# Kernel tuning notes

Measured on AMD Instinct MI355X. Metric: run time of the kernel, lower is better.

Reference implementation:

```python
import jax, jax.numpy as jnp
import numpy as np

B, N = 4, 2048
NUM_SHAPES = 16
EPS = 1e-5


def _angle(u, v):
    # u, v: [b, 3, n] -> angle via atan2(||u x v||, u.v), standard PPF angle
    s = jnp.linalg.norm(jnp.cross(u, v, axis=1), axis=1)
    c = jnp.sum(u * v, axis=1)
    return jnp.arctan2(s, c)


def _ppf(p1, p2, n1, n2):
    d = p2 - p1  # [b,3,n]
    return jnp.stack([_angle(n1, d), _angle(n2, d), _angle(n1, n2),
                      jnp.linalg.norm(d, axis=1)], axis=1)  # [b,4,n]


def _smlp(x, w, g, b):
    # 1x1 Conv1d (no bias; absorbed by BN) + BatchNorm1d (batch stats) + ReLU
    y = jnp.einsum('oc,bcn->bon', w, x)
    mu = y.mean(axis=(0, 2), keepdims=True)
    var = jnp.mean((y - mu) ** 2, axis=(0, 2), keepdims=True)
    y = (y - mu) * jax.lax.rsqrt(var + EPS) * g[None, :, None] + b[None, :, None]
    return jax.nn.relu(y)


def _forward(inputs, pf0_w, pf0_g, pf0_b, pf1_w, pf1_g, pf1_b,
             pf2_w, pf2_g, pf2_b, pf3_w, pf3_g, pf3_b,
             cls0_w, cls0_g, cls0_b, cls1_w, cls1_g, cls1_b,
             cls2_w, cls2_g, cls2_b, cls3_w, cls3_bias):
    one_hot = inputs[:, -NUM_SHAPES:, :]
    coords = inputs[:, :3, :]
    n = coords.shape[2]
    normals = inputs[:, 3:6, :]
    normals = normals / jnp.linalg.norm(normals, axis=1, keepdims=True)

    cc = coords.mean(axis=2, keepdims=True)          # [b,3,1]
    cn = normals.mean(axis=2, keepdims=True)         # [b,3,1]
    ncn = cn / jnp.linalg.norm(cn, axis=1, keepdims=True)

    old_ppfs = _ppf(jnp.broadcast_to(cc, coords.shape), coords,
                    jnp.broadcast_to(cn, coords.shape), normals)  # [b,4,n]

    nc = coords - cc
    dot = jnp.sum(nc * ncn, axis=1, keepdims=True)   # [b,1,n]
    proj = nc - dot * cn                              # [b,3,n] (unnormalized cn, as in source)
    P = proj.transpose(0, 2, 1)                       # [b,n,3]

    cos_a = jnp.einsum('bic,bjc->bij', P, P)          # [b,n,n]
    sin_a = jnp.linalg.norm(jnp.cross(P[:, :, None, :], P[:, None, :, :]), axis=-1)
    at = jnp.arctan2(sin_a, cos_a)
    at = jnp.where(at <= 1e-5, jnp.float32(100.0), at)
    # torch.median -> lower median: sorted index (n-1)//2
    alpha = jnp.sort(at, axis=2)[:, :, (n - 1) // 2]  # [b,n]

    feats = jnp.concatenate([old_ppfs, alpha[:, None, :]], axis=1)  # [b,5,n]

    outs = [one_hot]
    f = feats
    for w, g, b in [(pf0_w, pf0_g, pf0_b), (pf1_w, pf1_g, pf1_b),
                    (pf2_w, pf2_g, pf2_b), (pf3_w, pf3_g, pf3_b)]:
        f = _smlp(f, w, g, b)
        outs.append(f)
    outs.append(jnp.broadcast_to(jnp.max(f, axis=-1, keepdims=True), f.shape))
    x = jnp.concatenate(outs, axis=1)                 # [b,2384,n]

    for w, g, b in [(cls0_w, cls0_g, cls0_b), (cls1_w, cls1_g, cls1_b),
                    (cls2_w, cls2_g, cls2_b)]:
        x = _smlp(x, w, g, b)
    return jnp.einsum('oc,bcn->bon', cls3_w, x) + cls3_bias[None, :, None]


def setup_inputs() -> dict:
    key = jax.random.key(0)
    ks = jax.random.split(key, 12)
    inp = {"inputs": jax.random.normal(ks[0], (B, 3 + 3 + NUM_SHAPES, N), jnp.float32)}
    pf_dims = [(5, 64), (64, 128), (128, 128), (128, 1024)]
    for i, (ci, co) in enumerate(pf_dims):
        inp[f"pf{i}_w"] = jax.random.normal(ks[1 + i], (co, ci), jnp.float32) / np.sqrt(ci).astype(np.float32)
        inp[f"pf{i}_g"] = jnp.ones((co,), jnp.float32)
        inp[f"pf{i}_b"] = jnp.zeros((co,), jnp.float32)
    cls_dims = [(2384, 256), (256, 256), (256, 128)]
    for j, (ci, co) in enumerate(cls_dims):
        inp[f"cls{j}_w"] = jax.random.normal(ks[6 + j], (co, ci), jnp.float32) / np.sqrt(ci).astype(np.float32)
        inp[f"cls{j}_g"] = jnp.ones((co,), jnp.float32)
        inp[f"cls{j}_b"] = jnp.zeros((co,), jnp.float32)
    inp["cls3_w"] = jax.random.normal(ks[10], (50, 128), jnp.float32) / np.sqrt(128).astype(np.float32)
    inp["cls3_bias"] = jnp.zeros((50,), jnp.float32)
    return inp


def reference(inputs, pf0_w, pf0_g, pf0_b, pf1_w, pf1_g, pf1_b,
              pf2_w, pf2_g, pf2_b, pf3_w, pf3_g, pf3_b,
              cls0_w, cls0_g, cls0_b, cls1_w, cls1_g, cls1_b,
              cls2_w, cls2_g, cls2_b, cls3_w, cls3_bias):
    return _forward(inputs, pf0_w, pf0_g, pf0_b, pf1_w, pf1_g, pf1_b,
                    pf2_w, pf2_g, pf2_b, pf3_w, pf3_g, pf3_b,
                    cls0_w, cls0_g, cls0_b, cls1_w, cls1_g, cls1_b,
                    cls2_w, cls2_g, cls2_b, cls3_w, cls3_bias)
```

## Files before the change

### kernel.cpp

```cpp
#include <hip/hip_runtime.h>
#include <math.h>

#define BB 4
#define NN 2048
#define MM 8192
#define EPSF 1e-5f
#define LDC 1376

typedef _Float16 half8 __attribute__((ext_vector_type(8)));
typedef float f32x4 __attribute__((ext_vector_type(4)));

__device__ __forceinline__ unsigned short f2h(float x) {
    _Float16 h = (_Float16)x;
    return __builtin_bit_cast(unsigned short, h);
}
__device__ __forceinline__ float h2f(unsigned short u) {
    return (float)__builtin_bit_cast(_Float16, u);
}
__device__ __forceinline__ unsigned fflip(float x) {
    unsigned u = __builtin_bit_cast(unsigned, x);
    return (u >> 31) ? ~u : (u | 0x80000000u);
}
__device__ __forceinline__ float funflip(unsigned s) {
    unsigned u = (s >> 31) ? (s ^ 0x80000000u) : ~s;
    return __builtin_bit_cast(float, u);
}
#define FLIP_NEG_INF 0x007FFFFFu

__device__ __forceinline__ int wave_sum_dpp(int v) {
    v += __builtin_amdgcn_update_dpp(0, v, 0x111, 0xF, 0xF, true);
    v += __builtin_amdgcn_update_dpp(0, v, 0x112, 0xF, 0xF, true);
    v += __builtin_amdgcn_update_dpp(0, v, 0x114, 0xF, 0xF, true);
    v += __builtin_amdgcn_update_dpp(0, v, 0x118, 0xF, 0xF, true);
    v += __builtin_amdgcn_update_dpp(0, v, 0x142, 0xa, 0xF, true);
    v += __builtin_amdgcn_update_dpp(0, v, 0x143, 0xc, 0xF, true);
    return __builtin_amdgcn_readlane(v, 63);
}

__device__ __forceinline__ float angle3(float ux, float uy, float uz,
                                        float vx, float vy, float vz) {
    float crx = uy * vz - uz * vy;
    float cry = uz * vx - ux * vz;
    float crz = ux * vy - uy * vx;
    float s = sqrtf(crx * crx + cry * cry + crz * crz);
    float c = ux * vx + uy * vy + uz * vz;
    return atan2f(s, c);
}

__device__ __forceinline__ void bncoef(const float* __restrict__ sums,
                                       const float* __restrict__ g,
                                       const float* __restrict__ bb,
                                       int o, float& a, float& c) {
    float mu = sums[o] * (1.f / 8192.f);
    float var = sums[1024 + o] * (1.f / 8192.f) - mu * mu;
    var = fmaxf(var, 0.f);
    a = g[o] * (1.0f / sqrtf(var + EPSF));
    c = bb[o] - mu * a;
}

__global__ __launch_bounds__(256) void prep_k(const float* __restrict__ in,
                                              const float* __restrict__ w1, const float* __restrict__ w2,
                                              const float* __restrict__ w3, const float* __restrict__ w4,
                                              const float* __restrict__ w5, const float* __restrict__ w6,
                                              const float* __restrict__ w7,
                                              unsigned short* __restrict__ Wb,
                                              float* __restrict__ st,
                                              unsigned* __restrict__ zp,
                                              unsigned short* __restrict__ XCb) {
    int blk = blockIdx.x;
    int t = threadIdx.x;
    if (blk < 864) {
        int idx0 = blk * 1024 + t * 4;
        ushort4 r;
        unsigned short* rp = (unsigned short*)&r;
        #pragma unroll
        for (int e = 0; e < 4; ++e) {
            int idx = idx0 + e;
            unsigned short v;
            if (idx < 8192) v = f2h(w1[idx]);
            else if (idx < 24576) v = f2h(w2[idx - 8192]);
            else if (idx < 155648) v = f2h(w3[idx - 24576]);
            else if (idx < 507904) {
                int l = idx - 155648;
                int o = l / 1376, k = l - o * 1376;
                v = (k < 1360) ? f2h(w4[o * 2384 + k]) : (unsigned short)0;
            } else if (idx < 573440) v = f2h(w5[idx - 507904]);
            else if (idx < 606208) v = f2h(w6[idx - 573440]);
            else if (idx < 614400) {
                int l = idx - 606208;
                int o = l >> 7, k = l & 127;
                v = (o < 50) ? f2h(w7[o * 128 + k]) : (unsigned short)0;
            } else {
                int l = idx - 614400;
                int c = l >> 8, o = l & 255;
                v = (c < 1024) ? f2h(w4[o * 2384 + 1360 + c]) : (unsigned short)0;
            }
            rp[e] = v;
        }
        *(ushort4*)&Wb[idx0] = r;
    } else if (blk < 868) {
        int b = blk - 864;
        const float* base = in + (size_t)b * 22 * NN;
        float cs0 = 0.f, cs1 = 0.f, cs2 = 0.f, ns0 = 0.f, ns1 = 0.f, ns2 = 0.f;
        for (int n = t; n < NN; n += 256) {
            float cx = base[0 * NN + n], cy = base[1 * NN + n], cz = base[2 * NN + n];
            float nx = base[3 * NN + n], ny = base[4 * NN + n], nz = base[5 * NN + n];
            float inv = 1.0f / sqrtf(nx * nx + ny * ny + nz * nz);
            cs0 += cx; cs1 += cy; cs2 += cz;
            ns0 += nx * inv; ns1 += ny * inv; ns2 += nz * inv;
        }
        __shared__ float red[6][256];
        red[0][t] = cs0; red[1][t] = cs1; red[2][t] = cs2;
        red[3][t] = ns0; red[4][t] = ns1; red[5][t] = ns2;
        __syncthreads();
        for (int s = 128; s > 0; s >>= 1) {
            if (t < s) {
                #pragma unroll
                for (int i = 0; i < 6; ++i) red[i][t] += red[i][t + s];
            }
            __syncthreads();
        }
        if (t == 0) {
            float ccx = red[0][0] / (float)NN, ccy = red[1][0] / (float)NN, ccz = red[2][0] / (float)NN;
            float cnx = red[3][0] / (float)NN, cny = red[4][0] / (float)NN, cnz = red[5][0] / (float)NN;
            float inv = 1.0f / sqrtf(cnx * cnx + cny * cny + cnz * cnz);
            float* s9 = st + b * 16;
            s9[0] = ccx; s9[1] = ccy; s9[2] = ccz;
            s9[3] = cnx; s9[4] = cny; s9[5] = cnz;
            s9[6] = cnx * inv; s9[7] = cny * inv; s9[8] = cnz * inv;
        }
    } else if (blk < 944) {
        int idx = (blk - 868) * 256 + t;
        zp[idx] = (idx >= 14336 && idx < 18432) ? FLIP_NEG_INF : 0u;
    } else {
        int m = (blk - 944) * 256 + t;
        int b = m >> 11, n = m & (NN - 1);
        const float* src = in + (size_t)b * 22 * NN + 6 * NN + n;
        unsigned short vals[16];
        #pragma unroll
        for (int r = 0; r < 16; ++r) vals[r] = f2h(src[(size_t)r * NN]);
        ushort4* dst = (ushort4*)&XCb[(size_t)m * LDC];
        #pragma unroll
        for (int q = 0; q < 4; ++q)
            dst[q] = make_ushort4(vals[4 * q], vals[4 * q + 1], vals[4 * q + 2], vals[4 * q + 3]);
        ushort4 z = make_ushort4(0, 0, 0, 0);
        ushort4* pz = (ushort4*)&XCb[(size_t)m * LDC + 1360];
        pz[0] = z; pz[1] = z; pz[2] = z; pz[3] = z;
    }
}

__global__ __launch_bounds__(256) void point_k(const float* __restrict__ in,
                                               const float* __restrict__ st,
                                               float4* __restrict__ PQ,
                                               float* __restrict__ F0) {
    int idx = blockIdx.x * 256 + threadIdx.x;
    int b = idx >> 11, n = idx & (NN - 1);
    const float* base = in + (size_t)b * 22 * NN;
    const float* s9 = st + b * 16;
    float cx = base[0 * NN + n], cy = base[1 * NN + n], cz = base[2 * NN + n];
    float nx = base[3 * NN + n], ny = base[4 * NN + n], nz = base[5 * NN + n];
    float inv = 1.0f / sqrtf(nx * nx + ny * ny + nz * nz);
    nx *= inv; ny *= inv; nz *= inv;
    float ccx = s9[0], ccy = s9[1], ccz = s9[2];
    float cnx = s9[3], cny = s9[4], cnz = s9[5];
    float ex = s9[6], ey = s9[7], ez = s9[8];
    float dx = cx - ccx, dy = cy - ccy, dz = cz - ccz;
    F0[0 * MM + idx] = angle3(cnx, cny, cnz, dx, dy, dz);
    F0[1 * MM + idx] = angle3(nx, ny, nz, dx, dy, dz);
    F0[2 * MM + idx] = angle3(cnx, cny, cnz, nx, ny, nz);
    F0[3 * MM + idx] = sqrtf(dx * dx + dy * dy + dz * dz);
    float dot = dx * ex + dy * ey + dz * ez;
    float px = dx - dot * cnx;
    float py = dy - dot * cny;
    float pz = dz - dot * cnz;
    PQ[idx] = make_float4(px, py, pz, sqrtf(px * px + py * py + pz * pz));
}

__global__ __launch_bounds__(256) void alpha_k(const float4* __restrict__ PQ,
                                               float* __restrict__ F0) {
    int row = blockIdx.x * 4 + (threadIdx.x >> 6);
    int lane = threadIdx.x & 63;
    int b = row >> 11;
    const float4* base = PQ + (size_t)b * NN;
    float4 a = base[row & (NN - 1)];
    unsigned u[32];
    #pragma unroll
    for (int c = 0; c < 4; ++c) {
        #pragma unroll
        for (int j = 0; j < 8; ++j) {
            int s2 = c * 8 + j;
            float4 bv = base[s2 * 64 + lane];
            float cx = a.y * bv.z - a.z * bv.y;
            float cy = a.z * bv.x - a.x * bv.z;
            float cz = a.x * bv.y - a.y * bv.x;
            float ss = cx * cx + cy * cy + cz * cz;
            float dc = a.x * bv.x + a.y * bv.y + a.z * bv.z;
            float den = dc + a.w * bv.w;
            float rc = __builtin_amdgcn_rcpf(den);
            float key = ss * rc * rc;
            u[s2] = (key <= 2.5e-11f) ? 0x7F800000u : __float_as_uint(key);
        }
        asm volatile("" ::: "memory");
    }
    unsigned T = 0u;
    for (int bit = 30; bit >= 14; --bit) {
        unsigned c = T | (1u << bit);
        int s0 = 0, s1 = 0;
        #pragma unroll
        for (int q = 0; q < 8; ++q) {
            s0 += (int)__popcll(__ballot(u[16 + q] < c));
            s1 += (int)__popcll(__ballot(u[24 + q] < c));
        }
        int v0 = 0, v1 = 0, v2 = 0, v3 = 0;
        #pragma unroll
        for (int q = 0; q < 4; ++q) {
            v0 += (int)(u[q] < c);
            v1 += (int)(u[4 + q] < c);
            v2 += (int)(u[8 + q] < c);
            v3 += (int)(u[12 + q] < c);
        }
        int vsum = wave_sum_dpp(v0 + v1 + v2 + v3);
        if (vsum + s0 + s1 <= 1023) T = c;
    }
    if (lane == 0)
        F0[4 * MM + row] = 2.0f * atanf(sqrtf(__uint_as_float(T + 8192u)));
}

__global__ __launch_bounds__(256) void pf0s_k(const float* __restrict__ F0,
                                              const float* __restrict__ W,
                                              unsigned short* __restrict__ dst,
                                              float* __restrict__ sums) {
    __shared__ float ws[320];
    int t = threadIdx.x;
    for (int i = t; i < 320; i += 256) ws[i] = W[i];
    __syncthreads();
    int ol = t & 63, mg = t >> 6;
    int m0 = blockIdx.x * 512;
    float w0 = ws[ol * 5], w1 = ws[ol * 5 + 1], w2 = ws[ol * 5 + 2], w3 = ws[ol * 5 + 3], w4 = ws[ol * 5 + 4];
    float s = 0.f, q = 0.f;
    for (int i = 0; i < 128; ++i) {
        int m = m0 + i * 4 + mg;
        float y = w0 * F0[m] + w1 * F0[MM + m] + w2 * F0[2 * MM + m]
                + w3 * F0[3 * MM + m] + w4 * F0[4 * MM + m];
        dst[(size_t)m * LDC + ol] = f2h(y);
        s += y; q += y * y;
    }
    __shared__ float ls[4][64], lq[4][64];
    ls[mg][ol] = s; lq[mg][ol] = q;
    __syncthreads();
    if (mg == 0) {
        s = ls[0][ol] + ls[1][ol] + ls[2][ol] + ls[3][ol];
        q = lq[0][ol] + lq[1][ol] + lq[2][ol] + lq[3][ol];
        atomicAdd(&sums[ol], s);
        atomicAdd(&sums[1024 + ol], q);
    }
}

template<int MODE, int TRANS, int DOMAX>
__global__ __launch_bounds__(256) void mgemm3_k(const unsigned short* __restrict__ X, int ldx,
                                                const unsigned short* __restrict__ W, int ldw,
                                                unsigned short* __restrict__ Yh, int yld, int Co, int K, int kchunk,
                                                float* __restrict__ sums,
                                                const float* __restrict__ xs, const float* __restrict__ xg,
                                                const float* __restrict__ xb,
                                                const float4* __restrict__ AB4,
                                                unsigned* __restrict__ maxbu) {
    __shared__ unsigned short As[64 * 32];
    __shared__ unsigned short Bs[128 * 32];
    __shared__ float4 ABl[352];
    int t = threadIdx.x;
    int mBase = blockIdx.x * 64;
    int oBase = blockIdx.y * 128;
    int k0c = blockIdx.z * kchunk;
    int k1c = k0c + kchunk; if (k1c > K) k1c = K;
    if (TRANS == 1) {
        float* abf = (float*)ABl;
        for (int i = t; i < K; i += 256) {
            float a, c; bncoef(xs, xg, xb, i, a, c);
            abf[2 * i] = a; abf[2 * i + 1] = c;
        }
    } else if (TRANS == 2) {
        for (int i = t; i < k1c - k0c; i += 256) ABl[i] = AB4[k0c + i];
    }
    int lane = t & 63, w = t >> 6;
    int warpM = (w & 1) * 32, warpO = (w >> 1) * 64;
    f32x4 acc[2][4];
    #pragma unroll
    for (int i = 0; i < 2; ++i)
        #pragma unroll
        for (int j = 0; j < 4; ++j) acc[i][j] = (f32x4){0.f, 0.f, 0.f, 0.f};
    int lr = t >> 2;
    int lc = (t & 3) * 8;
    const unsigned short* Xp = X + (size_t)(mBase + lr) * ldx + lc;
    const unsigned short* Wp0 = W + (size_t)(oBase + lr) * ldw + lc;
    const unsigned short* Wp1 = W + (size_t)(oBase + lr + 64) * ldw + lc;
    int ar0 = (warpM + (lane & 15)) * 32 + (lane >> 4) * 8;
    int br0 = (warpO + (lane & 15)) * 32 + (lane >> 4) * 8;
    uint4 xa = *(const uint4*)(Xp + k0c);
    uint4 wb0 = *(const uint4*)(Wp0 + k0c);
    uint4 wb1 = *(const uint4*)(Wp1 + k0c);
    for (int k = k0c; k < k1c; k += 32) {
        __syncthreads();
        uint4 xc = xa;
        if (TRANS == 1) {
            const float* abf = (const float*)ABl;
            unsigned short* p = (unsigned short*)&xc;
            int kb = k + lc;
            #pragma unroll
            for (int e = 0; e < 8; ++e)
                p[e] = f2h(fmaxf(abf[2 * (kb + e)] * h2f(p[e]) + abf[2 * (kb + e) + 1], 0.f));
        } else if (TRANS == 2) {
            unsigned short* p = (unsigned short*)&xc;
            int kb = k + lc - k0c;
            #pragma unroll
            for (int e = 0; e < 8; ++e) {
                float4 qd = ABl[kb + e];
                p[e] = f2h(fmaxf(qd.x * h2f(p[e]) + qd.y, qd.z));
            }
        }
        *(uint4*)&As[lr * 32 + lc] = xc;
        *(uint4*)&Bs[lr * 32 + lc] = wb0;
        *(uint4*)&Bs[(lr + 64) * 32 + lc] = wb1;
        if (k + 32 < k1c) {
            xa = *(const uint4*)(Xp + k + 32);
            wb0 = *(const uint4*)(Wp0 + k + 32);
            wb1 = *(const uint4*)(Wp1 + k + 32);
        }
        __syncthreads();
        half8 a0 = __builtin_bit_cast(half8, *(const uint4*)&As[ar0]);
        half8 a1 = __builtin_bit_cast(half8, *(const uint4*)&As[ar0 + 16 * 32]);
        half8 b0 = __builtin_bit_cast(half8, *(const uint4*)&Bs[br0]);
        half8 b1 = __builtin_bit_cast(half8, *(const uint4*)&Bs[br0 + 16 * 32]);
        half8 b2 = __builtin_bit_cast(half8, *(const uint4*)&Bs[br0 + 32 * 32]);
        half8 b3 = __builtin_bit_cast(half8, *(const uint4*)&Bs[br0 + 48 * 32]);
        acc[0][0] = __builtin_amdgcn_mfma_f32_16x16x32_f16(a0, b0, acc[0][0], 0, 0, 0);
        acc[0][1] = __builtin_amdgcn_mfma_f32_16x16x32_f16(a0, b1, acc[0][1], 0, 0, 0);
        acc[0][2] = __builtin_amdgcn_mfma_f32_16x16x32_f16(a0, b2, acc[0][2], 0, 0, 0);
        acc[0][3] = __builtin_amdgcn_mfma_f32_16x16x32_f16(a0, b3, acc[0][3], 0, 0, 0);
        acc[1][0] = __builtin_amdgcn_mfma_f32_16x16x32_f16(a1, b0, acc[1][0], 0, 0, 0);
        acc[1][1] = __builtin_amdgcn_mfma_f32_16x16x32_f16(a1, b1, acc[1][1], 0, 0, 0);
        acc[1][2] = __builtin_amdgcn_mfma_f32_16x16x32_f16(a1, b2, acc[1][2], 0, 0, 0);
        acc[1][3] = __builtin_amdgcn_mfma_f32_16x16x32_f16(a1, b3, acc[1][3], 0, 0, 0);
    }
    unsigned short* Yp = Yh + (MODE == 2 ? (size_t)blockIdx.z * MM * yld : 0);
    #pragma unroll
    for (int i = 0; i < 2; ++i)
        #pragma unroll
        for (int j = 0; j < 4; ++j) {
            int m0 = mBase + warpM + i * 16 + (lane >> 4) * 4;
            int o = oBase + warpO + j * 16 + (lane & 15);
            #pragma unroll
            for (int r = 0; r < 4; ++r)
                Yp[(size_t)(m0 + r) * yld + o] = f2h(acc[i][j][r]);
        }
    if (MODE == 1) {
        __syncthreads();
        float* ssum = (float*)As;
        unsigned* smax = (unsigned*)As + 128;
        float* ssq = (float*)Bs;
        if (t < 128) { ssum[t] = 0.f; ssq[t] = 0.f; if (DOMAX) smax[t] = FLIP_NEG_INF; }
        __syncthreads();
        #pragma unroll
        for (int j = 0; j < 4; ++j) {
            int oc = warpO + j * 16 + (lane & 15);
            float s = 0.f, q = 0.f, mx = -__builtin_inff();
            #pragma unroll
            for (int i = 0; i < 2; ++i)
                #pragma unroll
                for (int r = 0; r < 4; ++r) {
                    float v = acc[i][j][r];
                    s += v; q += v * v; mx = fmaxf(mx, v);
                }
            atomicAdd(&ssum[oc], s);
            atomicAdd(&ssq[oc], q);
            if (DOMAX) atomicMax(&smax[oc], fflip(mx));
        }
        __syncthreads();
        if (t < 128) {
            atomicAdd(&sums[oBase + t], ssum[t]);
            atomicAdd(&sums[1024 + oBase + t], ssq[t]);
            if (DOMAX) atomicMax(&maxbu[(mBase >> 11) * 1024 + oBase + t], smax[t]);
        }
    }
}

template<int MODE, int TRANS>
__global__ __launch_bounds__(256) void mgemm64_k(const unsigned short* __restrict__ X, int ldx,
                                                 const unsigned short* __restrict__ W, int ldw,
                                                 void* __restrict__ Yv, int yld, int Co, int K,
                                                 float* __restrict__ sums,
                                                 const float* __restrict__ xs, const float* __restrict__ xg,
                                                 const float* __restrict__ xb) {
    __shared__ unsigned short As[64 * 32];
    __shared__ unsigned short Bs[64 * 32];
    __shared__ float ABl[512];
    int t = threadIdx.x;
    int mBase = blockIdx.x * 64;
    int oBase = blockIdx.y * 64;
    if (TRANS == 1) {
        for (int i = t; i < K; i += 256) {
            float a, c; bncoef(xs, xg, xb, i, a, c);
            ABl[2 * i] = a; ABl[2 * i + 1] = c;
        }
    }
    int lane = t & 63, w = t >> 6;
    int warpM = (w & 1) * 32, warpO = (w >> 1) * 32;
    f32x4 acc[2][2];
    #pragma unroll
    for (int i = 0; i < 2; ++i)
        #pragma unroll
        for (int j = 0; j < 2; ++j) acc[i][j] = (f32x4){0.f, 0.f, 0.f, 0.f};
    int lr = t >> 2;
    int lc = (t & 3) * 8;
    const unsigned short* Xp = X + (size_t)(mBase + lr) * ldx + lc;
    const unsigned short* Wp = W + (size_t)(oBase + lr) * ldw + lc;
    int ar0 = (warpM + (lane & 15)) * 32 + (lane >> 4) * 8;
    int br0 = (warpO + (lane & 15)) * 32 + (lane >> 4) * 8;
    uint4 xa = *(const uint4*)(Xp);
    uint4 wb = *(const uint4*)(Wp);
    for (int k = 0; k < K; k += 32) {
        __syncthreads();
        uint4 xc = xa;
        if (TRANS == 1) {
            unsigned short* p = (unsigned short*)&xc;
            int kb = k + lc;
            #pragma unroll
            for (int e = 0; e < 8; ++e)
                p[e] = f2h(fmaxf(ABl[2 * (kb + e)] * h2f(p[e]) + ABl[2 * (kb + e) + 1], 0.f));
        }
        *(uint4*)&As[lr * 32 + lc] = xc;
        *(uint4*)&Bs[lr * 32 + lc] = wb;
        if (k + 32 < K) {
            xa = *(const uint4*)(Xp + k + 32);
            wb = *(const uint4*)(Wp + k + 32);
        }
        __syncthreads();
        half8 a0 = __builtin_bit_cast(half8, *(const uint4*)&As[ar0]);
        half8 a1 = __builtin_bit_cast(half8, *(const uint4*)&As[ar0 + 16 * 32]);
        half8 b0 = __builtin_bit_cast(half8, *(const uint4*)&Bs[br0]);
        half8 b1 = __builtin_bit_cast(half8, *(const uint4*)&Bs[br0 + 16 * 32]);
        acc[0][0] = __builtin_amdgcn_mfma_f32_16x16x32_f16(a0, b0, acc[0][0], 0, 0, 0);
        acc[0][1] = __builtin_amdgcn_mfma_f32_16x16x32_f16(a0, b1, acc[0][1], 0, 0, 0);
        acc[1][0] = __builtin_amdgcn_mfma_f32_16x16x32_f16(a1, b0, acc[1][0], 0, 0, 0);
        acc[1][1] = __builtin_amdgcn_mfma_f32_16x16x32_f16(a1, b1, acc[1][1], 0, 0, 0);
    }
    if (MODE == 3) {
        float* outp = (float*)Yv;
        #pragma unroll
        for (int i = 0; i < 2; ++i)
            #pragma unroll
            for (int j = 0; j < 2; ++j) {
                int m0 = mBase + warpM + i * 16 + (lane >> 4) * 4;
                int o = oBase + warpO + j * 16 + (lane & 15);
                if (o < 50) {
                    int bb2 = m0 >> 11, n = m0 & (NN - 1);
                    float bi = sums[o];
                    float4 v = make_float4(acc[i][j][0] + bi, acc[i][j][1] + bi,
                                           acc[i][j][2] + bi, acc[i][j][3] + bi);
                    *(float4*)&outp[((size_t)bb2 * 50 + o) * NN + n] = v;
                }
            }
    } else {
        unsigned short* Yh = (unsigned short*)Yv;
        #pragma unroll
        for (int i = 0; i < 2; ++i)
            #pragma unroll
            for (int j = 0; j < 2; ++j) {
                int m0 = mBase + warpM + i * 16 + (lane >> 4) * 4;
                int o = oBase + warpO + j * 16 + (lane & 15);
                #pragma unroll
                for (int r = 0; r < 4; ++r)
                    Yh[(size_t)(m0 + r) * yld + o] = f2h(acc[i][j][r]);
            }
        __syncthreads();
        float* ssum = (float*)As;
        float* ssq = (float*)Bs;
        if (t < 64) { ssum[t] = 0.f; ssq[t] = 0.f; }
        __syncthreads();
        #pragma unroll
        for (int j = 0; j < 2; ++j) {
            int oc = warpO + j * 16 + (lane & 15);
            float s = 0.f, q = 0.f;
            #pragma unroll
            for (int i = 0; i < 2; ++i)
                #pragma unroll
                for (int r = 0; r < 4; ++r) { float v = acc[i][j][r]; s += v; q += v * v; }
            atomicAdd(&ssum[oc], s);
            atomicAdd(&ssq[oc], q);
        }
        __syncthreads();
        if (t < 64) {
            atomicAdd(&sums[oBase + t], ssum[t]);
            atomicAdd(&sums[1024 + oBase + t], ssq[t]);
        }
    }
}

__global__ __launch_bounds__(256) void abbuild_k(const float* __restrict__ SUMS,
                                                 const unsigned* __restrict__ MAXBu,
                                                 float4* __restrict__ AB4,
                                                 float* __restrict__ NMAXB,
                                                 const float* g0, const float* b0,
                                                 const float* g1, const float* b1,
                                                 const float* g2, const float* b2,
                                                 const float* g3, const float* b3) {
    int blk = blockIdx.x, t = threadIdx.x;
    if (blk < 6) {
        int ch = blk * 256 + t;
        if (ch >= 1376) return;
        float4 r;
        if (ch < 16) r = make_float4(1.f, 0.f, -__builtin_inff(), 0.f);
        else if (ch < 80) { float a, c; bncoef(SUMS, g0, b0, ch - 16, a, c); r = make_float4(a, c, 0.f, 0.f); }
        else if (ch < 208) { float a, c; bncoef(SUMS + 2048, g1, b1, ch - 80, a, c); r = make_float4(a, c, 0.f, 0.f); }
        else if (ch < 336) { float a, c; bncoef(SUMS + 4096, g2, b2, ch - 208, a, c); r = make_float4(a, c, 0.f, 0.f); }
        else if (ch < 1360) { float a, c; bncoef(SUMS + 6144, g3, b3, ch - 336, a, c); r = make_float4(a, c, 0.f, 0.f); }
        else r = make_float4(0.f, 0.f, 0.f, 0.f);
        AB4[ch] = r;
    } else {
        int idx = (blk - 6) * 256 + t;
        int c = idx & 1023;
        float a, cc; bncoef(SUMS + 6144, g3, b3, c, a, cc);
        float raw = funflip(MAXBu[idx]);
        NMAXB[idx] = fmaxf(a * raw + cc, 0.f);
    }
}

__global__ __launch_bounds__(256) void gemv_k(const unsigned short* __restrict__ Wmax,
                                              const float* __restrict__ nmax,
                                              float* __restrict__ contrib) {
    int b = blockIdx.x >> 3;
    int cc = (blockIdx.x & 7) * 128;
    int o = threadIdx.x;
    const float* mv = nmax + b * 1024 + cc;
    float acc = 0.f;
    for (int c = 0; c < 128; ++c)
        acc += h2f(Wmax[(size_t)(cc + c) * 256 + o]) * mv[c];
    atomicAdd(&contrib[b * 256 + o], acc);
}

__global__ __launch_bounds__(256) void red4stat_k(unsigned short* __restrict__ Yh,
                                                  const float* __restrict__ contrib,
                                                  float* __restrict__ sums) {
    int o0 = blockIdx.x * 64;
    int m0 = blockIdx.y * 128;
    int t = threadIdx.x, ol = t & 63, mg = t >> 6;
    int b = m0 >> 11;
    float cb = contrib[b * 256 + o0 + ol];
    const size_t stride = (size_t)MM * 256;
    float s = 0.f, q = 0.f;
    unsigned short* p = Yh + (size_t)(m0 + mg) * 256 + o0 + ol;
    for (int i = 0; i < 32; ++i) {
        unsigned short* pp = p + (size_t)i * 4 * 256;
        float v = h2f(pp[0]) + h2f(pp[stride]) + h2f(pp[2 * stride]) + h2f(pp[3 * stride]) + cb;
        pp[0] = f2h(v);
        s += v; q += v * v;
    }
    __shared__ float ls[4][64], lq[4][64];
    ls[mg][ol] = s; lq[mg][ol] = q;
    __syncthreads();
    if (mg == 0) {
        s = ls[0][ol] + ls[1][ol] + ls[2][ol] + ls[3][ol];
        q = lq[0][ol] + lq[1][ol] + lq[2][ol] + lq[3][ol];
        atomicAdd(&sums[o0 + ol], s);
        atomicAdd(&sums[1024 + o0 + ol], q);
    }
}

extern "C" void kernel_launch(void* const* d_in, const int* in_sizes, int n_in,
                              void* d_out, int out_size, void* d_ws, size_t ws_size,
                              hipStream_t stream) {
    const float* in = (const float*)d_in[0];
    const float* pf0_w = (const float*)d_in[1];
    const float* pf_g[4] = {(const float*)d_in[2], (const float*)d_in[5], (const float*)d_in[8], (const float*)d_in[11]};
    const float* pf_b[4] = {(const float*)d_in[3], (const float*)d_in[6], (const float*)d_in[9], (const float*)d_in[12]};
    const float* pf_w[4] = {(const float*)d_in[1], (const float*)d_in[4], (const float*)d_in[7], (const float*)d_in[10]};
    const float* cls_w[3] = {(const float*)d_in[13], (const float*)d_in[16], (const float*)d_in[19]};
    const float* cls_g[3] = {(const float*)d_in[14], (const float*)d_in[17], (const float*)d_in[20]};
    const float* cls_b[3] = {(const float*)d_in[15], (const float*)d_in[18], (const float*)d_in[21]};
    const float* cls3_w = (const float*)d_in[22];
    const float* cls3_bias = (const float*)d_in[23];
    float* out = (float*)d_out;

    char* wsb = (char*)d_ws;
    float* ST = (float*)(wsb + 0);
    float4* PQ = (float4*)(wsb + 256);
    float* F0 = (float*)(wsb + 131328);
    float* SUMS = (float*)(wsb + 295168);
    unsigned* MAXBu = (unsigned*)(wsb + 352512);
    float* CONTRIB = (float*)(wsb + 368896);
    float4* AB4 = (float4*)(wsb + 372992);
    float* NMAXB = (float*)(wsb + 395008);
    unsigned short* WB = (unsigned short*)(wsb + 411392);
    unsigned short* XCb = (unsigned short*)(wsb + 2180864);
    unsigned short* C1b = (unsigned short*)(wsb + 24725248);
    unsigned short* C2b = (unsigned short*)(wsb + 28919552);
    unsigned short* Yh = (unsigned short*)(wsb + 33113856);

    auto SL = [&](int s) { return SUMS + (size_t)s * 2048; };

    prep_k<<<976, 256, 0, stream>>>(in, pf_w[1], pf_w[2], pf_w[3], cls_w[0], cls_w[1], cls_w[2], cls3_w,
                                    WB, ST, (unsigned*)SUMS, XCb);
    point_k<<<MM / 256, 256, 0, stream>>>(in, ST, PQ, F0);
    alpha_k<<<MM / 4, 256, 0, stream>>>(PQ, F0);

    pf0s_k<<<16, 256, 0, stream>>>(F0, pf0_w, XCb + 16, SL(0));
    mgemm64_k<1, 1><<<dim3(128, 2), 256, 0, stream>>>(XCb + 16, LDC, WB, 64, XCb + 80, LDC, 128, 64,
                                                      SL(1), SL(0), pf_g[0], pf_b[0]);
    mgemm64_k<1, 1><<<dim3(128, 2), 256, 0, stream>>>(XCb + 80, LDC, WB + 8192, 128, XCb + 208, LDC, 128, 128,
                                                      SL(2), SL(1), pf_g[1], pf_b[1]);
    mgemm3_k<1, 1, 1><<<dim3(128, 8, 1), 256, 0, stream>>>(XCb + 208, LDC, WB + 24576, 128, XCb + 336, LDC,
                                                           1024, 128, 128, SL(3), SL(2), pf_g[2], pf_b[2],
                                                           AB4, MAXBu);
    abbuild_k<<<22, 256, 0, stream>>>(SUMS, MAXBu, AB4, NMAXB,
                                      pf_g[0], pf_b[0], pf_g[1], pf_b[1], pf_g[2], pf_b[2], pf_g[3], pf_b[3]);
    gemv_k<<<32, 256, 0, stream>>>(WB + 614400, NMAXB, CONTRIB);
    mgemm3_k<2, 2, 0><<<dim3(128, 2, 4), 256, 0, stream>>>(XCb, LDC, WB + 155648, 1376, Yh, 256,
                                                           256, 1376, 352, SL(4), nullptr, nullptr, nullptr,
                                                           AB4, MAXBu);
    red4stat_k<<<dim3(4, 64), 256, 0, stream>>>(Yh, CONTRIB, SL(4));
    mgemm64_k<1, 1><<<dim3(128, 4), 256, 0, stream>>>(Yh, 256, WB + 507904, 256, C1b, 256, 256, 256,
                                                      SL(5), SL(4), cls_g[0], cls_b[0]);
    mgemm64_k<1, 1><<<dim3(128, 2), 256, 0, stream>>>(C1b, 256, WB + 507904 + 65536, 256, C2b, 128, 128, 256,
                                                      SL(6), SL(5), cls_g[1], cls_b[1]);
    mgemm64_k<3, 1><<<dim3(128, 1), 256, 0, stream>>>(C2b, 128, WB + 606208, 128, (void*)out, 0, 64, 128,
                                                      (float*)cls3_bias, SL(6), cls_g[2], cls_b[2]);

    (void)in_sizes; (void)n_in; (void)out_size; (void)ws_size;
}
```

Measured before the change: 179.9 us.

## Pack alpha keys as fp16 pairs and fuse BN-max with gemv kernel

The median-angle kernel now stores each tan^2 key as fp16, packing two per 32-bit register. This halves register use, and the radix select over the 15 fp16 bits needs fewer ballot and compare steps. The median is then taken as the midpoint of the chosen fp16 bucket. Separately, the BN coefficient/max normalisation and the gemv are merged into one kernel through shared memory, which removes a launch and an intermediate buffer. The fp16 quantisation reduces the precision of alpha, which may affect accuracy.

Result: no change. 178.6 us (-0.7%).

```diff
diff --git a/kernel.cpp b/kernel.cpp
--- a/kernel.cpp
+++ b/kernel.cpp
@@ -183,47 +183,64 @@
     int b = row >> 11;
     const float4* base = PQ + (size_t)b * NN;
     float4 a = base[row & (NN - 1)];
-    unsigned u[32];
+    unsigned u[16];
     #pragma unroll
     for (int c = 0; c < 4; ++c) {
         #pragma unroll
-        for (int j = 0; j < 8; ++j) {
-            int s2 = c * 8 + j;
-            float4 bv = base[s2 * 64 + lane];
-            float cx = a.y * bv.z - a.z * bv.y;
-            float cy = a.z * bv.x - a.x * bv.z;
-            float cz = a.x * bv.y - a.y * bv.x;
-            float ss = cx * cx + cy * cy + cz * cz;
-            float dc = a.x * bv.x + a.y * bv.y + a.z * bv.z;
-            float den = dc + a.w * bv.w;
-            float rc = __builtin_amdgcn_rcpf(den);
-            float key = ss * rc * rc;
-            u[s2] = (key <= 2.5e-11f) ? 0x7F800000u : __float_as_uint(key);
+        for (int j = 0; j < 4; ++j) {
+            int s2 = c * 8 + j * 2;
+            float4 bv0 = base[s2 * 64 + lane];
+            float4 bv1 = base[(s2 + 1) * 64 + lane];
+            float k0, k1;
+            {
+                float cx = a.y * bv0.z - a.z * bv0.y;
+                float cy = a.z * bv0.x - a.x * bv0.z;
+                float cz = a.x * bv0.y - a.y * bv0.x;
+                float ss = cx * cx + cy * cy + cz * cz;
+                float dc = a.x * bv0.x + a.y * bv0.y + a.z * bv0.z;
+                float den = dc + a.w * bv0.w;
+                float rc = __builtin_amdgcn_rcpf(den);
+                k0 = ss * rc * rc;
+                if (k0 <= 2.5e-11f) k0 = __builtin_inff();
+            }
+            {
+                float cx = a.y * bv1.z - a.z * bv1.y;
+                float cy = a.z * bv1.x - a.x * bv1.z;
+                float cz = a.x * bv1.y - a.y * bv1.x;
+                float ss = cx * cx + cy * cy + cz * cz;
+                float dc = a.x * bv1.x + a.y * bv1.y + a.z * bv1.z;
+                float den = dc + a.w * bv1.w;
+                float rc = __builtin_amdgcn_rcpf(den);
+                k1 = ss * rc * rc;
+                if (k1 <= 2.5e-11f) k1 = __builtin_inff();
+            }
+            u[c * 4 + j] = (unsigned)f2h(k0) | ((unsigned)f2h(k1) << 16);
         }
         asm volatile("" ::: "memory");
     }
     unsigned T = 0u;
-    for (int bit = 30; bit >= 14; --bit) {
+    for (int bit = 14; bit >= 0; --bit) {
         unsigned c = T | (1u << bit);
         int s0 = 0, s1 = 0;
         #pragma unroll
         for (int q = 0; q < 8; ++q) {
-            s0 += (int)__popcll(__ballot(u[16 + q] < c));
-            s1 += (int)__popcll(__ballot(u[24 + q] < c));
-        }
-        int v0 = 0, v1 = 0, v2 = 0, v3 = 0;
-        #pragma unroll
-        for (int q = 0; q < 4; ++q) {
-            v0 += (int)(u[q] < c);
-            v1 += (int)(u[4 + q] < c);
-            v2 += (int)(u[8 + q] < c);
-            v3 += (int)(u[12 + q] < c);
-        }
-        int vsum = wave_sum_dpp(v0 + v1 + v2 + v3);
+            s0 += (int)__popcll(__ballot((u[8 + q] & 0xFFFFu) < c));
+            s1 += (int)__popcll(__ballot((u[8 + q] >> 16) < c));
+        }
+        int v0 = 0, v1 = 0;
+        #pragma unroll
+        for (int q = 0; q < 8; ++q) {
+            v0 += (int)((u[q] & 0xFFFFu) < c);
+            v1 += (int)((u[q] >> 16) < c);
+        }
+        int vsum = wave_sum_dpp(v0 + v1);
         if (vsum + s0 + s1 <= 1023) T = c;
     }
-    if (lane == 0)
-        F0[4 * MM + row] = 2.0f * atanf(sqrtf(__uint_as_float(T + 8192u)));
+    if (lane == 0) {
+        float lo = h2f((unsigned short)T);
+        float hi = h2f((unsigned short)(T + 1));
+        F0[4 * MM + row] = 2.0f * atanf(sqrtf(0.5f * (lo + hi)));
+    }
 }
 
 __global__ __launch_bounds__(256) void pf0s_k(const float* __restrict__ F0,
@@ -496,14 +513,15 @@
     }
 }
 
-__global__ __launch_bounds__(256) void abbuild_k(const float* __restrict__ SUMS,
-                                                 const unsigned* __restrict__ MAXBu,
-                                                 float4* __restrict__ AB4,
-                                                 float* __restrict__ NMAXB,
-                                                 const float* g0, const float* b0,
-                                                 const float* g1, const float* b1,
-                                                 const float* g2, const float* b2,
-                                                 const float* g3, const float* b3) {
+__global__ __launch_bounds__(256) void abgemv_k(const float* __restrict__ SUMS,
+                                                const unsigned* __restrict__ MAXBu,
+                                                float4* __restrict__ AB4,
+                                                const unsigned short* __restrict__ Wmax,
+                                                float* __restrict__ contrib,
+                                                const float* g0, const float* b0,
+                                                const float* g1, const float* b1,
+                                                const float* g2, const float* b2,
+                                                const float* g3, const float* b3) {
     int blk = blockIdx.x, t = threadIdx.x;
     if (blk < 6) {
         int ch = blk * 256 + t;
@@ -517,25 +535,23 @@
         else r = make_float4(0.f, 0.f, 0.f, 0.f);
         AB4[ch] = r;
     } else {
-        int idx = (blk - 6) * 256 + t;
-        int c = idx & 1023;
-        float a, cc; bncoef(SUMS + 6144, g3, b3, c, a, cc);
-        float raw = funflip(MAXBu[idx]);
-        NMAXB[idx] = fmaxf(a * raw + cc, 0.f);
-    }
-}
-
-__global__ __launch_bounds__(256) void gemv_k(const unsigned short* __restrict__ Wmax,
-                                              const float* __restrict__ nmax,
-                                              float* __restrict__ contrib) {
-    int b = blockIdx.x >> 3;
-    int cc = (blockIdx.x & 7) * 128;
-    int o = threadIdx.x;
-    const float* mv = nmax + b * 1024 + cc;
-    float acc = 0.f;
-    for (int c = 0; c < 128; ++c)
-        acc += h2f(Wmax[(size_t)(cc + c) * 256 + o]) * mv[c];
-    atomicAdd(&contrib[b * 256 + o], acc);
+        int i = blk - 6;
+        int b = i >> 3;
+        int cc = (i & 7) * 128;
+        __shared__ float nm[128];
+        if (t < 128) {
+            int c = cc + t;
+            float a, cf; bncoef(SUMS + 6144, g3, b3, c, a, cf);
+            float raw = funflip(MAXBu[b * 1024 + c]);
+            nm[t] = fmaxf(a * raw + cf, 0.f);
+        }
+        __syncthreads();
+        int o = t;
+        float acc = 0.f;
+        for (int c = 0; c < 128; ++c)
+            acc += h2f(Wmax[(size_t)(cc + c) * 256 + o]) * nm[c];
+        atomicAdd(&contrib[b * 256 + o], acc);
+    }
 }
 
 __global__ __launch_bounds__(256) void red4stat_k(unsigned short* __restrict__ Yh,
@@ -589,7 +605,6 @@
     unsigned* MAXBu = (unsigned*)(wsb + 352512);
     float* CONTRIB = (float*)(wsb + 368896);
     float4* AB4 = (float4*)(wsb + 372992);
-    float* NMAXB = (float*)(wsb + 395008);
     unsigned short* WB = (unsigned short*)(wsb + 411392);
     unsigned short* XCb = (unsigned short*)(wsb + 2180864);
     unsigned short* C1b = (unsigned short*)(wsb + 24725248);
@@ -611,9 +626,8 @@
     mgemm3_k<1, 1, 1><<<dim3(128, 8, 1), 256, 0, stream>>>(XCb + 208, LDC, WB + 24576, 128, XCb + 336, LDC,
                                                            1024, 128, 128, SL(3), SL(2), pf_g[2], pf_b[2],
                                                            AB4, MAXBu);
-    abbuild_k<<<22, 256, 0, stream>>>(SUMS, MAXBu, AB4, NMAXB,
-                                      pf_g[0], pf_b[0], pf_g[1], pf_b[1], pf_g[2], pf_b[2], pf_g[3], pf_b[3]);
-    gemv_k<<<32, 256, 0, stream>>>(WB + 614400, NMAXB, CONTRIB);
+    abgemv_k<<<38, 256, 0, stream>>>(SUMS, MAXBu, AB4, WB + 614400, CONTRIB,
+                                     pf_g[0], pf_b[0], pf_g[1], pf_b[1], pf_g[2], pf_b[2], pf_g[3], pf_b[3]);
     mgemm3_k<2, 2, 0><<<dim3(128, 2, 4), 256, 0, stream>>>(XCb, LDC, WB + 155648, 1376, Yh, 256,
                                                            256, 1376, 352, SL(4), nullptr, nullptr, nullptr,
                                                            AB4, MAXBu);
```
